# Optimization experiments

Measured on AMD Instinct MI355X. Metric: run time of the kernel, lower is better.

## Reference

```python
import jax, jax.numpy as jnp
import numpy as np

B, H, W, D = 8, 32, 32, 512
NH = 8
DK = DV = 512
DKH = DK // NH
DVH = DV // NH


def setup_inputs() -> dict:
    key = jax.random.key(0)
    ks = jax.random.split(key, 16)
    s = 0.02
    return {
        "q": jax.random.normal(ks[0], (B, H, W, D), dtype=jnp.float32),
        "k": jax.random.normal(ks[1], (B, H, W, D), dtype=jnp.float32),
        "q_mask": jax.random.randint(ks[2], (B, H, W), 0, 2).astype(bool),
        "k_mask": jax.random.randint(ks[3], (B, H, W), 0, 2).astype(bool),
        "pos_logits": jax.random.normal(ks[4], (B, H, W, H, W), dtype=jnp.float32),
        "Wq": jax.random.normal(ks[5], (D, DK), dtype=jnp.float32) * s,
        "bq": jnp.zeros((DK,), dtype=jnp.float32),
        "Wk": jax.random.normal(ks[6], (D, DK), dtype=jnp.float32) * s,
        "bk": jnp.zeros((DK,), dtype=jnp.float32),
        "Wv": jax.random.normal(ks[7], (DK, DV), dtype=jnp.float32) * s,
        "bv": jnp.zeros((DV,), dtype=jnp.float32),
        "Wo": jax.random.normal(ks[8], (DV, D), dtype=jnp.float32) * s,
        "bo": jnp.zeros((D,), dtype=jnp.float32),
    }


def _split_heads(x, nh):
    b, h, w, d = x.shape
    return x.reshape(b, h, w, nh, d // nh).transpose(0, 3, 1, 2, 4)  # [B,Nh,H,W,dh]


def reference(q, k, q_mask, k_mask, pos_logits, Wq, bq, Wk, bk, Wv, bv, Wo, bo):
    b, h, w, d = q.shape
    qp = (q @ Wq + bq) * (DKH ** -0.5)
    kp = k @ Wk + bk
    vp = kp @ Wv + bv  # faithful quirk: v = projv(projk(k))
    qs = _split_heads(qp, NH)  # [B,Nh,H,W,dkh]
    ks_ = _split_heads(kp, NH)
    vs = _split_heads(vp, NH)  # [B,Nh,H,W,dvh]
    # additive mask: -inf where exactly one of q_mask[i,j], k_mask[k,l] is set
    xor = q_mask[:, :, :, None, None] ^ k_mask[:, None, None, :, :]  # [B,H,W,H,W]
    attn_mask = jnp.where(xor, -jnp.inf, 0.0)[:, None]  # [B,1,H,W,H,W]
    con = jnp.einsum('bhijd,bhkld->bhijkl', qs, ks_)  # [B,Nh,H,W,H,W]
    logits = attn_mask + con + pos_logits[:, None]
    weights = jax.nn.softmax(logits.reshape(b, NH, h, w, h * w), axis=-1)
    weights = weights.reshape(b, NH, h, w, h, w)
    attn = jnp.einsum('bhijkl,bhkld->bhijd', weights, vs)  # [B,Nh,H,W,dvh]
    attn = attn.transpose(0, 2, 3, 1, 4).reshape(b, h, w, NH * DVH)
    return attn @ Wo + bo  # dropout is identity at inference
```

## Files before the change

kernel.cpp:

```cpp
#include <hip/hip_runtime.h>
#include <hip/hip_bf16.h>
#include <math.h>

#define TOK 8192
#define DMODEL 512
#define SEQ 1024
#define NHEADS 8
#define DH 64
#define NBATCH 8

typedef __attribute__((ext_vector_type(8))) short short8v;
typedef __attribute__((ext_vector_type(4))) float f32x4;
typedef __attribute__((ext_vector_type(4))) int i32x4;

#define MFMA16(a, b, c) __builtin_amdgcn_mfma_f32_16x16x32_bf16(a, b, c, 0, 0, 0)

#define SW(row, c) ((c) ^ (((row) & 7) << 3))

__device__ __forceinline__ unsigned short f2bf(float x) {
  __hip_bfloat16 h = __float2bfloat16(x);
  unsigned short u;
  __builtin_memcpy(&u, &h, 2);
  return u;
}
__device__ __forceinline__ unsigned int pk2(float a, float b) {
  return (unsigned int)f2bf(a) | ((unsigned int)f2bf(b) << 16);
}

__global__ __launch_bounds__(256) void wtr4_kernel(
    const float* __restrict__ W0, const float* __restrict__ W1,
    const float* __restrict__ W2, const float* __restrict__ W3,
    unsigned short* __restrict__ T0, unsigned short* __restrict__ T1,
    unsigned short* __restrict__ T2, unsigned short* __restrict__ T3) {
  __shared__ unsigned short tile[64][72];
  const int z = blockIdx.z;
  const float* W = (z == 0) ? W0 : (z == 1) ? W1 : (z == 2) ? W2 : W3;
  unsigned short* Wt = (z == 0) ? T0 : (z == 1) ? T1 : (z == 2) ? T2 : T3;
  const int kt = blockIdx.x, nt = blockIdx.y;
  const int t = threadIdx.x, r = t >> 2, c0 = (t & 3) * 16;
  const float* src = W + (size_t)(kt * 64 + r) * 512 + nt * 64 + c0;
  short8v v0, v1;
#pragma unroll
  for (int e = 0; e < 4; ++e) {
    float4 f = *reinterpret_cast<const float4*>(src + e * 4);
    short* dstv = (e < 2) ? (short*)&v0 : (short*)&v1;
    dstv[(e & 1) * 4 + 0] = (short)f2bf(f.x);
    dstv[(e & 1) * 4 + 1] = (short)f2bf(f.y);
    dstv[(e & 1) * 4 + 2] = (short)f2bf(f.z);
    dstv[(e & 1) * 4 + 3] = (short)f2bf(f.w);
  }
  *reinterpret_cast<short8v*>(&tile[r][c0]) = v0;
  *reinterpret_cast<short8v*>(&tile[r][c0 + 8]) = v1;
  __syncthreads();
  short8v o0, o1;
#pragma unroll
  for (int e = 0; e < 8; ++e) o0[e] = (short)tile[c0 + e][r];
#pragma unroll
  for (int e = 0; e < 8; ++e) o1[e] = (short)tile[c0 + 8 + e][r];
  unsigned short* dst = Wt + (size_t)(nt * 64 + r) * 512 + kt * 64 + c0;
  *reinterpret_cast<short8v*>(dst) = o0;
  *reinterpret_cast<short8v*>(dst + 8) = o1;
}

template <int AF32, int OUTMODE>
__device__ __forceinline__ void gemm_body(
    const void* __restrict__ Ap, const unsigned short* __restrict__ Wt,
    const float* __restrict__ bias, float scale, void* __restrict__ Cout) {
  __shared__ unsigned short Asl[128 * 64];
  __shared__ unsigned short Bsl[128 * 64];
  const int t = threadIdx.x;
  const int w = t >> 6, lane = t & 63, li = lane & 15, lg = lane >> 4;
  const int wr = w >> 1, wc = w & 1;
  const int rowBase = blockIdx.y * 128, colBase = blockIdx.x * 128;

  f32x4 zero4 = {0.f, 0.f, 0.f, 0.f};
  f32x4 acc[4][4];
#pragma unroll
  for (int mi = 0; mi < 4; ++mi)
#pragma unroll
    for (int nj = 0; nj < 4; ++nj) acc[mi][nj] = zero4;

  const int sr = t >> 1, sh = (t & 1) * 32;
  const float* af32base =
      AF32 ? reinterpret_cast<const float*>(Ap) + (size_t)(rowBase + sr) * 512 + sh : nullptr;
  const unsigned short* abf16base =
      AF32 ? nullptr
           : reinterpret_cast<const unsigned short*>(Ap) + (size_t)(rowBase + sr) * 512 + sh;
  const unsigned short* bbase = Wt + (size_t)(colBase + sr) * 512 + sh;
  int sdst[4];
#pragma unroll
  for (int qq = 0; qq < 4; ++qq) sdst[qq] = sr * 64 + SW(sr, sh + qq * 8);

  {
    if (AF32) {
#pragma unroll
      for (int qq = 0; qq < 4; ++qq) {
        float4 f0 = *reinterpret_cast<const float4*>(af32base + qq * 8);
        float4 f1 = *reinterpret_cast<const float4*>(af32base + qq * 8 + 4);
        short8v o;
        o[0] = (short)f2bf(f0.x); o[1] = (short)f2bf(f0.y);
        o[2] = (short)f2bf(f0.z); o[3] = (short)f2bf(f0.w);
        o[4] = (short)f2bf(f1.x); o[5] = (short)f2bf(f1.y);
        o[6] = (short)f2bf(f1.z); o[7] = (short)f2bf(f1.w);
        *reinterpret_cast<short8v*>(&Asl[sdst[qq]]) = o;
      }
    } else {
#pragma unroll
      for (int qq = 0; qq < 4; ++qq)
        *reinterpret_cast<short8v*>(&Asl[sdst[qq]]) =
            *reinterpret_cast<const short8v*>(abf16base + qq * 8);
    }
#pragma unroll
    for (int qq = 0; qq < 4; ++qq)
      *reinterpret_cast<short8v*>(&Bsl[sdst[qq]]) =
          *reinterpret_cast<const short8v*>(bbase + qq * 8);
  }
  __syncthreads();

  for (int kt = 0; kt < 8; ++kt) {
    const int knext = (kt + 1) * 64;

    float4 paf[8];
    short8v pab[4];
    short8v pbb[4];
    if (kt < 7) {
      if (AF32) {
#pragma unroll
        for (int qq = 0; qq < 4; ++qq) {
          paf[2 * qq]     = *reinterpret_cast<const float4*>(af32base + knext + qq * 8);
          paf[2 * qq + 1] = *reinterpret_cast<const float4*>(af32base + knext + qq * 8 + 4);
        }
      } else {
#pragma unroll
        for (int qq = 0; qq < 4; ++qq)
          pab[qq] = *reinterpret_cast<const short8v*>(abf16base + knext + qq * 8);
      }
#pragma unroll
      for (int qq = 0; qq < 4; ++qq)
        pbb[qq] = *reinterpret_cast<const short8v*>(bbase + knext + qq * 8);
    }

#pragma unroll
    for (int kk = 0; kk < 2; ++kk) {
      short8v af[4], bf[4];
#pragma unroll
      for (int mi = 0; mi < 4; ++mi) {
        const int ra = wr * 64 + mi * 16 + li;
        af[mi] = *reinterpret_cast<short8v*>(&Asl[ra * 64 + SW(ra, kk * 32 + lg * 8)]);
      }
#pragma unroll
      for (int nj = 0; nj < 4; ++nj) {
        const int rb = wc * 64 + nj * 16 + li;
        bf[nj] = *reinterpret_cast<short8v*>(&Bsl[rb * 64 + SW(rb, kk * 32 + lg * 8)]);
      }
#pragma unroll
      for (int mi = 0; mi < 4; ++mi)
#pragma unroll
        for (int nj = 0; nj < 4; ++nj) acc[mi][nj] = MFMA16(af[mi], bf[nj], acc[mi][nj]);
    }

    if (kt < 7) {
      __syncthreads();
      if (AF32) {
#pragma unroll
        for (int qq = 0; qq < 4; ++qq) {
          const float4 f0 = paf[2 * qq], f1 = paf[2 * qq + 1];
          short8v o;
          o[0] = (short)f2bf(f0.x); o[1] = (short)f2bf(f0.y);
          o[2] = (short)f2bf(f0.z); o[3] = (short)f2bf(f0.w);
          o[4] = (short)f2bf(f1.x); o[5] = (short)f2bf(f1.y);
          o[6] = (short)f2bf(f1.z); o[7] = (short)f2bf(f1.w);
          *reinterpret_cast<short8v*>(&Asl[sdst[qq]]) = o;
        }
      } else {
#pragma unroll
        for (int qq = 0; qq < 4; ++qq)
          *reinterpret_cast<short8v*>(&Asl[sdst[qq]]) = pab[qq];
      }
#pragma unroll
      for (int qq = 0; qq < 4; ++qq)
        *reinterpret_cast<short8v*>(&Bsl[sdst[qq]]) = pbb[qq];
      __syncthreads();
    }
  }

#pragma unroll
  for (int nj = 0; nj < 4; ++nj) {
    const int col = colBase + wc * 64 + nj * 16 + li;
    const float bv = bias[col];
#pragma unroll
    for (int mi = 0; mi < 4; ++mi) {
      const int row0 = rowBase + wr * 64 + mi * 16 + lg * 4;
      if (OUTMODE == 2) {
        const int hh = col >> 6, dd = col & 63;
        const int bb = row0 >> 10, jj = row0 & 1023;
        unsigned short* dst =
            reinterpret_cast<unsigned short*>(Cout) +
            ((size_t)((bb * 8 + hh) * 64 + dd)) * SEQ + jj;
        float v0 = (acc[mi][nj][0] + bv) * scale;
        float v1 = (acc[mi][nj][1] + bv) * scale;
        float v2 = (acc[mi][nj][2] + bv) * scale;
        float v3 = (acc[mi][nj][3] + bv) * scale;
        *reinterpret_cast<uint2*>(dst) = make_uint2(pk2(v0, v1), pk2(v2, v3));
      } else {
#pragma unroll
        for (int rr = 0; rr < 4; ++rr) {
          const int row = row0 + rr;
          const float v = (acc[mi][nj][rr] + bv) * scale;
          if (OUTMODE == 1)
            reinterpret_cast<float*>(Cout)[(size_t)row * 512 + col] = v;
          else
            reinterpret_cast<unsigned short*>(Cout)[(size_t)row * 512 + col] = f2bf(v);
        }
      }
    }
  }
}

__global__ __launch_bounds__(256) void gemm_qk(
    const float* __restrict__ q, const float* __restrict__ k,
    const unsigned short* __restrict__ Wqt, const unsigned short* __restrict__ Wkt,
    const float* __restrict__ bq, const float* __restrict__ bk,
    unsigned short* __restrict__ qpb, unsigned short* __restrict__ kpb) {
  const int z = blockIdx.z;
  const void* A = z ? (const void*)k : (const void*)q;
  const unsigned short* Wt = z ? Wkt : Wqt;
  const float* bias = z ? bk : bq;
  const float scale = z ? 1.0f : 0.125f;
  void* C = z ? (void*)kpb : (void*)qpb;
  gemm_body<1, 0>(A, Wt, bias, scale, C);
}

__global__ __launch_bounds__(256) void gemm_vp(
    const unsigned short* __restrict__ kpb, const unsigned short* __restrict__ Wvt,
    const float* __restrict__ bv, unsigned short* __restrict__ vtb) {
  gemm_body<0, 2>(kpb, Wvt, bv, 1.0f, vtb);
}

__global__ __launch_bounds__(256) void gemm_out(
    const unsigned short* __restrict__ attnb, const unsigned short* __restrict__ Wot,
    const float* __restrict__ bo, float* __restrict__ out) {
  gemm_body<0, 1>(attnb, Wot, bo, 1.0f, out);
}

__global__ __launch_bounds__(512, 4) void attn_mfma(
    const unsigned short* __restrict__ qp, const unsigned short* __restrict__ kp,
    const unsigned short* __restrict__ vt, const float* __restrict__ pos,
    const int* __restrict__ qmask, const int* __restrict__ kmask,
    unsigned short* __restrict__ outb) {
  const int bx = blockIdx.x;
  const int qc = bx >> 6, h = (bx >> 3) & 7, b = bx & 7;
  const int t = threadIdx.x, w = t >> 6, lane = t & 63, li = lane & 15, lg = lane >> 4;
  const int qrow = qc * 128 + w * 16;

  __shared__ unsigned short Kl[64 * 64];
  __shared__ unsigned short Vl[64 * 64];
  __shared__ unsigned short Pl[8][16 * 64];

  const size_t qg = (size_t)(b * SEQ + qrow + li) * DMODEL + h * DH;
  const short8v qf0 = *reinterpret_cast<const short8v*>(qp + qg + lg * 8);
  const short8v qf1 = *reinterpret_cast<const short8v*>(qp + qg + 32 + lg * 8);
  const int qmv = qmask[b * SEQ + qrow + li];

  f32x4 zero4 = {0.f, 0.f, 0.f, 0.f};
  f32x4 acc_o[4];
#pragma unroll
  for (int n = 0; n < 4; ++n) acc_o[n] = zero4;
  f32x4 psv = zero4;

  const int srow = t >> 3, schk = (t & 7) * 8;
  const unsigned short* kgp = kp + (size_t)(b * SEQ + srow) * DMODEL + h * DH + schk;
  const unsigned short* vgp = vt + ((size_t)((b * 8 + h) * 64) + srow) * SEQ + schk;
  const int sldst = srow * 64 + SW(srow, schk);

  const float* posb = pos + (size_t)(b * SEQ + qrow + li) * SEQ;
  const int* kmb = kmask + b * SEQ;

  int kofsA[4], kofsB[4], pofsW[4];
#pragma unroll
  for (int n = 0; n < 4; ++n) {
    const int rk = n * 16 + li;
    kofsA[n] = rk * 64 + SW(rk, lg * 8);
    kofsB[n] = rk * 64 + SW(rk, 32 + lg * 8);
    pofsW[n] = li * 64 + SW(li, n * 16 + lg * 4);
  }
  const int pofsR0 = li * 64 + SW(li, lg * 8);
  const int pofsR1 = li * 64 + SW(li, 32 + lg * 8);

  {
    short8v kr = *reinterpret_cast<const short8v*>(kgp);
    short8v vr = *reinterpret_cast<const short8v*>(vgp);
    *reinterpret_cast<short8v*>(&Kl[sldst]) = kr;
    *reinterpret_cast<short8v*>(&Vl[sldst]) = vr;
  }
  __syncthreads();

  for (int kt = 0; kt < 16; ++kt) {
    const int kbase = kt * 64;

    short8v kr, vr;
    if (kt < 15) {
      kr = *reinterpret_cast<const short8v*>(kgp + (size_t)(kbase + 64) * DMODEL);
      vr = *reinterpret_cast<const short8v*>(vgp + kbase + 64);
    }

    f32x4 pvn[4];
#pragma unroll
    for (int n = 0; n < 4; ++n) {
      f32x4 pv = *reinterpret_cast<const f32x4*>(posb + kbase + n * 16 + lg * 4);
      i32x4 km = *reinterpret_cast<const i32x4*>(kmb + kbase + n * 16 + lg * 4);
#pragma unroll
      for (int r = 0; r < 4; ++r) {
        float v = pv[r] - 16.0f;
        if ((qmv != 0) != (km[r] != 0)) v = -1e30f;
        pvn[n][r] = v;
      }
    }

    f32x4 x4[4];
    __builtin_amdgcn_s_setprio(1);
#pragma unroll
    for (int n = 0; n < 4; ++n) {
      short8v kfa = *reinterpret_cast<short8v*>(&Kl[kofsA[n]]);
      short8v kfb = *reinterpret_cast<short8v*>(&Kl[kofsB[n]]);
      x4[n] = MFMA16(kfa, qf0, zero4);
      x4[n] = MFMA16(kfb, qf1, x4[n]);
    }
    __builtin_amdgcn_s_setprio(0);

#pragma unroll
    for (int n = 0; n < 4; ++n) {
#pragma unroll
      for (int r = 0; r < 4; ++r) {
        const float p = __expf(x4[n][r] + pvn[n][r]);
        x4[n][r] = p;
      }
      psv += x4[n];
      *reinterpret_cast<uint2*>(&Pl[w][pofsW[n]]) =
          make_uint2(pk2(x4[n][0], x4[n][1]), pk2(x4[n][2], x4[n][3]));
    }
    asm volatile("s_waitcnt lgkmcnt(0)" ::: "memory");
    __builtin_amdgcn_sched_barrier(0);
    const short8v pf0 = *reinterpret_cast<short8v*>(&Pl[w][pofsR0]);
    const short8v pf1 = *reinterpret_cast<short8v*>(&Pl[w][pofsR1]);

    __builtin_amdgcn_s_setprio(1);
#pragma unroll
    for (int n = 0; n < 4; ++n) {
      short8v vfa = *reinterpret_cast<short8v*>(&Vl[kofsA[n]]);
      short8v vfb = *reinterpret_cast<short8v*>(&Vl[kofsB[n]]);
      acc_o[n] = MFMA16(pf0, vfa, acc_o[n]);
      acc_o[n] = MFMA16(pf1, vfb, acc_o[n]);
    }
    __builtin_amdgcn_s_setprio(0);

    if (kt < 15) {
      __syncthreads();
      *reinterpret_cast<short8v*>(&Kl[sldst]) = kr;
      *reinterpret_cast<short8v*>(&Vl[sldst]) = vr;
      __syncthreads();
    }
  }

  float lsum = (psv[0] + psv[1]) + (psv[2] + psv[3]);
  lsum += __shfl_xor(lsum, 16);
  lsum += __shfl_xor(lsum, 32);
  const float linv = 1.f / lsum;
  float lb[4];
#pragma unroll
  for (int r = 0; r < 4; ++r) lb[r] = __shfl(linv, lg * 4 + r, 16);
  unsigned short* ob = outb + (size_t)(b * SEQ + qrow) * DMODEL + h * DH;
#pragma unroll
  for (int n = 0; n < 4; ++n)
#pragma unroll
    for (int r = 0; r < 4; ++r)
      ob[(size_t)(lg * 4 + r) * DMODEL + n * 16 + li] = f2bf(acc_o[n][r] * lb[r]);
}

extern "C" void kernel_launch(void* const* d_in, const int* in_sizes, int n_in,
                              void* d_out, int out_size, void* d_ws, size_t ws_size,
                              hipStream_t stream) {
  const float* q   = (const float*)d_in[0];
  const float* k   = (const float*)d_in[1];
  const int*   qm  = (const int*)d_in[2];
  const int*   km  = (const int*)d_in[3];
  const float* pos = (const float*)d_in[4];
  const float* Wq  = (const float*)d_in[5];
  const float* bq  = (const float*)d_in[6];
  const float* Wk  = (const float*)d_in[7];
  const float* bk  = (const float*)d_in[8];
  const float* Wv  = (const float*)d_in[9];
  const float* bv  = (const float*)d_in[10];
  const float* Wo  = (const float*)d_in[11];
  const float* bo  = (const float*)d_in[12];
  float* out = (float*)d_out;

  char* ws = (char*)d_ws;
  const size_t MB8 = (size_t)TOK * DMODEL * 2;
  unsigned short* qpb   = (unsigned short*)(ws);
  unsigned short* kpb   = (unsigned short*)(ws + 1 * MB8);
  unsigned short* attnb = (unsigned short*)(ws + 2 * MB8);
  unsigned short* vtb   = (unsigned short*)(ws + 3 * MB8);
  unsigned short* Wqt   = (unsigned short*)(ws + 4 * MB8);
  unsigned short* Wkt   = Wqt + (size_t)512 * 512;
  unsigned short* Wvt   = Wkt + (size_t)512 * 512;
  unsigned short* Wot   = Wvt + (size_t)512 * 512;

  hipLaunchKernelGGL(wtr4_kernel, dim3(8, 8, 4), dim3(256), 0, stream,
                     Wq, Wk, Wv, Wo, Wqt, Wkt, Wvt, Wot);

  const dim3 ggrid(DMODEL / 128, TOK / 128);
  hipLaunchKernelGGL(gemm_qk, dim3(4, 64, 2), dim3(256), 0, stream,
                     q, k, Wqt, Wkt, bq, bk, qpb, kpb);
  hipLaunchKernelGGL(gemm_vp, ggrid, dim3(256), 0, stream, kpb, Wvt, bv, vtb);

  hipLaunchKernelGGL(attn_mfma, dim3(512), dim3(512), 0, stream,
                     qpb, kpb, vtb, pos, qm, km, attnb);

  hipLaunchKernelGGL(gemm_out, ggrid, dim3(256), 0, stream, attnb, Wot, bo, out);
}
```

Before: 114.6 us.

## Split attention over key dimension into two halves with separate merge kernel

Splits the attention kernel's key loop into two halves (split-K / flash-decoding style), doubling the grid from 512 to 1024 blocks. Each half writes unnormalised fp32 partial outputs and row sums to workspace. A new merge kernel adds the halves, normalises and writes the bf16 result. This raises parallelism and occupancy on the 256-CU GPU, at the cost of extra fp32 traffic (about 32 MB written and read) and one more launch. Because the softmax uses a fixed offset instead of a running max, the partial sums can be added directly.

```diff
diff --git a/kernel.cpp b/kernel.cpp
--- a/kernel.cpp
+++ b/kernel.cpp
@@ -247,11 +247,12 @@
     const unsigned short* __restrict__ qp, const unsigned short* __restrict__ kp,
     const unsigned short* __restrict__ vt, const float* __restrict__ pos,
     const int* __restrict__ qmask, const int* __restrict__ kmask,
-    unsigned short* __restrict__ outb) {
+    float* __restrict__ num, float* __restrict__ lp) {
   const int bx = blockIdx.x;
-  const int qc = bx >> 6, h = (bx >> 3) & 7, b = bx & 7;
+  const int s = bx >> 9, qc = (bx >> 6) & 7, h = (bx >> 3) & 7, b = bx & 7;
   const int t = threadIdx.x, w = t >> 6, lane = t & 63, li = lane & 15, lg = lane >> 4;
   const int qrow = qc * 128 + w * 16;
+  const int koff = s * 512;
 
   __shared__ unsigned short Kl[64 * 64];
   __shared__ unsigned short Vl[64 * 64];
@@ -269,12 +270,14 @@
   f32x4 psv = zero4;
 
   const int srow = t >> 3, schk = (t & 7) * 8;
-  const unsigned short* kgp = kp + (size_t)(b * SEQ + srow) * DMODEL + h * DH + schk;
-  const unsigned short* vgp = vt + ((size_t)((b * 8 + h) * 64) + srow) * SEQ + schk;
+  const unsigned short* kgp =
+      kp + (size_t)(b * SEQ + koff + srow) * DMODEL + h * DH + schk;
+  const unsigned short* vgp =
+      vt + ((size_t)((b * 8 + h) * 64) + srow) * SEQ + koff + schk;
   const int sldst = srow * 64 + SW(srow, schk);
 
-  const float* posb = pos + (size_t)(b * SEQ + qrow + li) * SEQ;
-  const int* kmb = kmask + b * SEQ;
+  const float* posb = pos + (size_t)(b * SEQ + qrow + li) * SEQ + koff;
+  const int* kmb = kmask + b * SEQ + koff;
 
   int kofsA[4], kofsB[4], pofsW[4];
 #pragma unroll
@@ -295,11 +298,11 @@
   }
   __syncthreads();
 
-  for (int kt = 0; kt < 16; ++kt) {
+  for (int kt = 0; kt < 8; ++kt) {
     const int kbase = kt * 64;
 
     short8v kr, vr;
-    if (kt < 15) {
+    if (kt < 7) {
       kr = *reinterpret_cast<const short8v*>(kgp + (size_t)(kbase + 64) * DMODEL);
       vr = *reinterpret_cast<const short8v*>(vgp + kbase + 64);
     }
@@ -354,7 +357,7 @@
     }
     __builtin_amdgcn_s_setprio(0);
 
-    if (kt < 15) {
+    if (kt < 7) {
       __syncthreads();
       *reinterpret_cast<short8v*>(&Kl[sldst]) = kr;
       *reinterpret_cast<short8v*>(&Vl[sldst]) = vr;
@@ -365,16 +368,38 @@
   float lsum = (psv[0] + psv[1]) + (psv[2] + psv[3]);
   lsum += __shfl_xor(lsum, 16);
   lsum += __shfl_xor(lsum, 32);
-  const float linv = 1.f / lsum;
-  float lb[4];
-#pragma unroll
-  for (int r = 0; r < 4; ++r) lb[r] = __shfl(linv, lg * 4 + r, 16);
-  unsigned short* ob = outb + (size_t)(b * SEQ + qrow) * DMODEL + h * DH;
+  if (lg == 0) lp[((size_t)s * 8 + h) * TOK + b * SEQ + qrow + li] = lsum;
+  float* ob = num + (size_t)s * TOK * 512 + (size_t)(b * SEQ + qrow) * 512 + h * DH;
 #pragma unroll
   for (int n = 0; n < 4; ++n)
 #pragma unroll
     for (int r = 0; r < 4; ++r)
-      ob[(size_t)(lg * 4 + r) * DMODEL + n * 16 + li] = f2bf(acc_o[n][r] * lb[r]);
+      ob[(size_t)(lg * 4 + r) * 512 + n * 16 + li] = acc_o[n][r];
+}
+
+__global__ __launch_bounds__(256) void attn_merge(
+    const float* __restrict__ num, const float* __restrict__ lp,
+    unsigned short* __restrict__ attnb) {
+  const int gid = blockIdx.x * 256 + threadIdx.x;
+  const int token = gid >> 6;
+  const int rem = gid & 63, h = rem >> 3, d0 = (rem & 7) * 8;
+  const size_t off = (size_t)token * 512 + h * 64 + d0;
+  const float4* n0 = reinterpret_cast<const float4*>(num + off);
+  const float4* n1 = reinterpret_cast<const float4*>(num + (size_t)TOK * 512 + off);
+  const float l0 = lp[(size_t)h * TOK + token];
+  const float l1 = lp[((size_t)8 + h) * TOK + token];
+  const float inv = 1.0f / (l0 + l1);
+  float4 a0 = n0[0], a1 = n0[1], b0 = n1[0], b1 = n1[1];
+  short8v o;
+  o[0] = (short)f2bf((a0.x + b0.x) * inv);
+  o[1] = (short)f2bf((a0.y + b0.y) * inv);
+  o[2] = (short)f2bf((a0.z + b0.z) * inv);
+  o[3] = (short)f2bf((a0.w + b0.w) * inv);
+  o[4] = (short)f2bf((a1.x + b1.x) * inv);
+  o[5] = (short)f2bf((a1.y + b1.y) * inv);
+  o[6] = (short)f2bf((a1.z + b1.z) * inv);
+  o[7] = (short)f2bf((a1.w + b1.w) * inv);
+  *reinterpret_cast<short8v*>(attnb + off) = o;
 }
 
 extern "C" void kernel_launch(void* const* d_in, const int* in_sizes, int n_in,
@@ -397,11 +422,14 @@
 
   char* ws = (char*)d_ws;
   const size_t MB8 = (size_t)TOK * DMODEL * 2;
+  const size_t MB16 = (size_t)TOK * DMODEL * 4;
   unsigned short* qpb   = (unsigned short*)(ws);
-  unsigned short* kpb   = (unsigned short*)(ws + 1 * MB8);
-  unsigned short* attnb = (unsigned short*)(ws + 2 * MB8);
-  unsigned short* vtb   = (unsigned short*)(ws + 3 * MB8);
-  unsigned short* Wqt   = (unsigned short*)(ws + 4 * MB8);
+  unsigned short* attnb = qpb;
+  unsigned short* kpb   = (unsigned short*)(ws + MB8);
+  unsigned short* vtb   = (unsigned short*)(ws + 2 * MB8);
+  float* num            = (float*)(ws + 3 * MB8);
+  float* lp             = (float*)(ws + 3 * MB8 + 2 * MB16);
+  unsigned short* Wqt   = (unsigned short*)(ws + 3 * MB8 + 2 * MB16 + 16 * TOK * 4);
   unsigned short* Wkt   = Wqt + (size_t)512 * 512;
   unsigned short* Wvt   = Wkt + (size_t)512 * 512;
   unsigned short* Wot   = Wvt + (size_t)512 * 512;
@@ -414,8 +442,11 @@
                      q, k, Wqt, Wkt, bq, bk, qpb, kpb);
   hipLaunchKernelGGL(gemm_vp, ggrid, dim3(256), 0, stream, kpb, Wvt, bv, vtb);
 
-  hipLaunchKernelGGL(attn_mfma, dim3(512), dim3(512), 0, stream,
-                     qpb, kpb, vtb, pos, qm, km, attnb);
+  hipLaunchKernelGGL(attn_mfma, dim3(1024), dim3(512), 0, stream,
+                     qpb, kpb, vtb, pos, qm, km, num, lp);
+
+  hipLaunchKernelGGL(attn_merge, dim3(TOK * 64 / 256), dim3(256), 0, stream,
+                     num, lp, attnb);
 
   hipLaunchKernelGGL(gemm_out, ggrid, dim3(256), 0, stream, attnb, Wot, bo, out);
 }
```

New measurement: 126.4 us. +10.3%, slower.
